# Optimization experiments

Measured on AMD Instinct MI355X. Metric: run time of the kernel, lower is better.

The kernel has to match this reference:

```python
import jax, jax.numpy as jnp
import numpy as np

NUM_EMBEDDINGS = 1024
EMBEDDING_DIM = 256
COMMITMENT_COST = 0.25
EPS_NORM = 1e-12  # F.normalize eps


def _l2_normalize(x, axis=-1):
    n = jnp.sqrt(jnp.sum(x * x, axis=axis, keepdims=True))
    return x / jnp.maximum(n, EPS_NORM)


def setup_inputs() -> dict:
    key = jax.random.key(0)
    k_in, k_w = jax.random.split(key)
    inputs = jax.random.normal(k_in, (16, 2048, 256), dtype=jnp.float32)
    # nn.Embedding weight initialized uniform(-1/K, 1/K)
    weight = jax.random.uniform(
        k_w, (NUM_EMBEDDINGS, EMBEDDING_DIM), dtype=jnp.float32,
        minval=-1.0 / NUM_EMBEDDINGS, maxval=1.0 / NUM_EMBEDDINGS)
    return {"inputs": inputs, "weight": weight}


def reference(inputs, weight):
    # inputs: [B, T, D]  weight: [K, D]
    B, T, D = inputs.shape
    K = weight.shape[0]

    x = jax.lax.stop_gradient(inputs)
    # cosine distance: normalized dot products  [B, T, K]
    distances = jnp.einsum(
        "btd,kd->btk", _l2_normalize(x), _l2_normalize(weight))

    encoding_indices = jnp.argmax(distances, axis=-1)            # [B, T]
    encodings = jax.nn.one_hot(encoding_indices, K, dtype=jnp.float32)  # [B, T, K]

    # one-hot matmul with codebook == gather
    quantized = jnp.take(weight, encoding_indices, axis=0)       # [B, T, D]

    e_latent_loss = COMMITMENT_COST * jnp.mean(
        (jax.lax.stop_gradient(quantized) - inputs) ** 2)
    q_latent_loss = jnp.mean((quantized - x) ** 2)

    # straight-through estimator
    quantized_st = inputs + jax.lax.stop_gradient(quantized - inputs)

    avg_probs = jnp.mean(encodings, axis=0)                      # [T, K]
    perplexity = jnp.exp(-jnp.sum(avg_probs * jnp.log(avg_probs + 1e-10)))

    # eval path (3D input): contra_loss = 0.0, no EMA/anchor update
    return (quantized_st,
            encoding_indices[..., None],
            q_latent_loss,
            e_latent_loss,
            perplexity,
            encodings)
```

## Files before the change

### kernel.cpp

```cpp
#include <hip/hip_runtime.h>
#include <math.h>
#include <float.h>

#define NUM_EMB   1024
#define DIM       256
#define BATCH     16
#define TLEN      2048
#define NTOK      (BATCH * TLEN)
#define QUANT_N   (NTOK * DIM)

#define QUANT_OFF 0
#define IDX_OFF   QUANT_N
#define QLOSS_OFF (IDX_OFF + NTOK)
#define ELOSS_OFF (QLOSS_OFF + 1)
#define PERP_OFF  (QLOSS_OFF + 2)
#define ENC_OFF   (QLOSS_OFF + 3)

typedef _Float16 f16;
typedef f16   f16x4 __attribute__((ext_vector_type(4)));
typedef f16   f16x8 __attribute__((ext_vector_type(8)));
typedef float f32x4 __attribute__((ext_vector_type(4)));

#define WS_XS_BYTE      0u
#define WS_WSP_BYTE     33554432u
#define WS_CNT_BYTE     34603008u
#define WS_WIN_BYTE     42991616u
#define WS_ACC_BYTE     43253760u
#define WS_NEED         (43253760u + 64u)

#define LWS_WHAT_BYTE   0
#define LWS_CNT_BYTE    1048576
#define LWS_ACC_BYTE    9437184

__device__ __forceinline__ void gl2lds16(const void* g, void* l) {
    __builtin_amdgcn_global_load_lds(
        (const __attribute__((address_space(1))) void*)g,
        (__attribute__((address_space(3))) void*)l, 16, 0, 0);
}


__global__ void k_zero_big(int4* __restrict__ counts4, int4* __restrict__ win4,
                           double* __restrict__ acc) {
    int i = blockIdx.x * blockDim.x + threadIdx.x;
    if (i < 524288) counts4[i] = make_int4(0, 0, 0, 0);
    else            win4[i - 524288] = make_int4(0, 0, 0, 0);
    if (i == 0) { acc[0] = 0.0; acc[1] = 0.0; }
}

__global__ void k_split_x(const float4* __restrict__ x4, f16* __restrict__ Xs) {
    int i = blockIdx.x * 256 + threadIdx.x;
    int row = i >> 6;
    int c4  = i & 63;
    float4 v = x4[i];
    f16 h0 = (f16)v.x, h1 = (f16)v.y, h2 = (f16)v.z, h3 = (f16)v.w;
    f16 l0 = (f16)(v.x - (float)h0), l1 = (f16)(v.y - (float)h1);
    f16 l2 = (f16)(v.z - (float)h2), l3 = (f16)(v.w - (float)h3);
    f16x4 hv = {h0, h1, h2, h3}, lv = {l0, l1, l2, l3};
    *(f16x4*)&Xs[(size_t)row * 512 + c4 * 4]       = hv;
    *(f16x4*)&Xs[(size_t)row * 512 + 256 + c4 * 4] = lv;
}

__global__ void k_norm_w_split(const float* __restrict__ w, f16* __restrict__ Ws) {
    int k = blockIdx.x;
    int lane = threadIdx.x;
    float4 v = ((const float4*)(w + (size_t)k * DIM))[lane];
    float ss = v.x * v.x + v.y * v.y + v.z * v.z + v.w * v.w;
    #pragma unroll
    for (int off = 32; off > 0; off >>= 1) ss += __shfl_down(ss, off);
    ss = __shfl(ss, 0);
    float denom = fmaxf(sqrtf(ss), 1e-12f);
    float a = v.x / denom, b = v.y / denom, c = v.z / denom, d = v.w / denom;
    f16 h0 = (f16)a, h1 = (f16)b, h2 = (f16)c, h3 = (f16)d;
    f16 l0 = (f16)(a - (float)h0), l1 = (f16)(b - (float)h1);
    f16 l2 = (f16)(c - (float)h2), l3 = (f16)(d - (float)h3);
    f16x4 hv = {h0, h1, h2, h3}, lv = {l0, l1, l2, l3};
    *(f16x4*)&Ws[(size_t)k * 512 + lane * 4]       = hv;
    *(f16x4*)&Ws[(size_t)k * 512 + 256 + lane * 4] = lv;
}

__global__ __launch_bounds__(256)
void k_gemm(const f16* __restrict__ Xs,
            const f16* __restrict__ Ws,
            unsigned long long* __restrict__ winners)
{
    __shared__ f16 As[128 * 32];
    __shared__ f16 Bs[128 * 32];
    __shared__ float redV[128][33];
    __shared__ int   redK[128][33];

    const int tid  = threadIdx.x;
    const int w    = tid >> 6, lane = tid & 63;
    const int tb   = blockIdx.x & 255;
    const int pg   = blockIdx.x >> 8;
    const int tok0 = tb * 128;
    const int wr   = w >> 1, wc = w & 1;
    const int quad = lane >> 4, l16 = lane & 15;

    const int stC0  = (w * 2) * 64 + lane;
    const int srow0 = stC0 >> 2, skc0 = (stC0 & 3) * 16;
    const int stC1  = stC0 + 64;
    const int srow1 = stC1 >> 2, skc1 = (stC1 & 3) * 16;

    for (int panel = 0; panel < 2; ++panel) {
        const int cw0 = (pg * 2 + panel) * 128;
        f32x4 acc[4][4];
        #pragma unroll
        for (int mi = 0; mi < 4; ++mi)
            #pragma unroll
            for (int ni = 0; ni < 4; ++ni)
                acc[mi][ni] = (f32x4){0.f, 0.f, 0.f, 0.f};

        const char* Xb = (const char*)Xs + (size_t)tok0 * 1024;
        const char* Wb = (const char*)Ws + (size_t)cw0 * 1024;

        for (int ks = 0; ks < 24; ++ks) {
            const int g = ks >> 3, r = ks & 7;
            const int akoff = ((g == 2) ? 512 : 0) + r * 64;
            const int bkoff = ((g == 1) ? 512 : 0) + r * 64;
            __syncthreads();
            gl2lds16(Xb + (size_t)srow0 * 1024 + akoff + skc0, (char*)As + (w * 2 + 0) * 1024);
            gl2lds16(Xb + (size_t)srow1 * 1024 + akoff + skc1, (char*)As + (w * 2 + 1) * 1024);
            gl2lds16(Wb + (size_t)srow0 * 1024 + bkoff + skc0, (char*)Bs + (w * 2 + 0) * 1024);
            gl2lds16(Wb + (size_t)srow1 * 1024 + bkoff + skc1, (char*)Bs + (w * 2 + 1) * 1024);
            __syncthreads();

            f16x8 af[4], bf[4];
            #pragma unroll
            for (int mi = 0; mi < 4; ++mi)
                af[mi] = *(const f16x8*)&As[(wr * 64 + mi * 16 + l16) * 32 + quad * 8];
            #pragma unroll
            for (int ni = 0; ni < 4; ++ni)
                bf[ni] = *(const f16x8*)&Bs[(wc * 64 + ni * 16 + l16) * 32 + quad * 8];
            #pragma unroll
            for (int mi = 0; mi < 4; ++mi)
                #pragma unroll
                for (int ni = 0; ni < 4; ++ni)
                    acc[mi][ni] = __builtin_amdgcn_mfma_f32_16x16x32_f16(
                        af[mi], bf[ni], acc[mi][ni], 0, 0, 0);
        }

        #pragma unroll
        for (int mi = 0; mi < 4; ++mi)
            #pragma unroll
            for (int rr = 0; rr < 4; ++rr) {
                float bv = acc[mi][0][rr]; int bk = cw0 + wc * 64 + l16;
                #pragma unroll
                for (int ni = 1; ni < 4; ++ni) {
                    float v = acc[mi][ni][rr];
                    int  kk = cw0 + wc * 64 + ni * 16 + l16;
                    if (v > bv) { bv = v; bk = kk; }
                }
                const int row = wr * 64 + mi * 16 + quad * 4 + rr;
                const int cg  = wc * 16 + l16;
                if (panel == 0) { redV[row][cg] = bv; redK[row][cg] = bk; }
                else if (bv > redV[row][cg]) { redV[row][cg] = bv; redK[row][cg] = bk; }
            }
    }
    __syncthreads();
    if (tid < 128) {
        float bv = redV[tid][0]; int bk = redK[tid][0];
        #pragma unroll 4
        for (int g2 = 1; g2 < 32; ++g2) {
            float v = redV[tid][g2]; int kk = redK[tid][g2];
            if (v > bv || (v == bv && kk < bk)) { bv = v; bk = kk; }
        }
        unsigned int ub = __float_as_uint(bv);
        ub = (ub & 0x80000000u) ? ~ub : (ub | 0x80000000u);
        unsigned long long key =
            ((unsigned long long)ub << 32) | (unsigned int)(1023 - bk);
        atomicMax(&winners[tok0 + tid], key);
    }
}

__global__ __launch_bounds__(256)
void k_epilogue(const float* __restrict__ x, const float* __restrict__ w,
                const unsigned long long* __restrict__ winners,
                float* __restrict__ out, int* __restrict__ counts,
                double* __restrict__ acc)
{
    const int wv = threadIdx.x >> 6, lane = threadIdx.x & 63;
    const int base = blockIdx.x * 32 + wv * 8;
    float mse = 0.0f;
    for (int t = 0; t < 8; ++t) {
        const int n = base + t;
        const int idx = 1023 - (int)(winners[n] & 1023u);
        float4 wvv = *(const float4*)(w + (size_t)idx * DIM + lane * 4);
        float4 xv  = *(const float4*)(x + (size_t)n * DIM + lane * 4);
        float dx = wvv.x - xv.x, dy = wvv.y - xv.y, dz = wvv.z - xv.z, dw2 = wvv.w - xv.w;
        mse += dx * dx + dy * dy + dz * dz + dw2 * dw2;
        *(float4*)(out + QUANT_OFF + (size_t)n * DIM + lane * 4) = wvv;
        if (lane == 0) {
            out[IDX_OFF + n] = (float)idx;
            atomicAdd(&counts[(n & (TLEN - 1)) * NUM_EMB + idx], 1);
        }
        float* enc = out + ENC_OFF + (size_t)n * NUM_EMB;
        #pragma unroll
        for (int s = 0; s < 4; ++s) {
            int kbase = s * 256 + lane * 4;
            float4 e;
            e.x = (kbase + 0 == idx) ? 1.0f : 0.0f;
            e.y = (kbase + 1 == idx) ? 1.0f : 0.0f;
            e.z = (kbase + 2 == idx) ? 1.0f : 0.0f;
            e.w = (kbase + 3 == idx) ? 1.0f : 0.0f;
            *(float4*)(enc + kbase) = e;
        }
    }
    #pragma unroll
    for (int off = 32; off > 0; off >>= 1) mse += __shfl_down(mse, off);
    if (lane == 0) atomicAdd(&acc[0], (double)mse);
}

__global__ void k_entropy(const int* __restrict__ counts, double* __restrict__ acc) {
    const int tid = blockIdx.x * blockDim.x + threadIdx.x;
    const int stride = gridDim.x * blockDim.x;
    float s = 0.0f;
    for (int e = tid; e < TLEN * NUM_EMB; e += stride) {
        int c = counts[e];
        if (c > 0) {
            float p = (float)c * 0.0625f;
            s += p * logf(p + 1e-10f);
        }
    }
    #pragma unroll
    for (int off = 32; off > 0; off >>= 1) s += __shfl_down(s, off);
    __shared__ float wsum[4];
    int lane = threadIdx.x & 63, wave = threadIdx.x >> 6;
    if (lane == 0) wsum[wave] = s;
    __syncthreads();
    if (threadIdx.x == 0) atomicAdd(&acc[1], (double)(wsum[0] + wsum[1] + wsum[2] + wsum[3]));
}

__global__ void k_final(const double* __restrict__ acc, float* __restrict__ out) {
    float mse_mean = (float)(acc[0] / (double)QUANT_N);
    out[QLOSS_OFF] = mse_mean;
    out[ELOSS_OFF] = 0.25f * mse_mean;
    float arg = -(float)acc[1];
    out[PERP_OFF] = (arg < 87.0f) ? expf(arg) : 3.0e38f;
}

__global__ void k_zero_legacy(int4* __restrict__ counts4, double* __restrict__ acc) {
    int i = blockIdx.x * blockDim.x + threadIdx.x;
    counts4[i] = make_int4(0, 0, 0, 0);
    if (i == 0) { acc[0] = 0.0; acc[1] = 0.0; }
}

__global__ void k_norm_w_legacy(const float* __restrict__ w, float* __restrict__ w_hat) {
    int k = blockIdx.x, lane = threadIdx.x;
    float4 v = ((const float4*)(w + (size_t)k * DIM))[lane];
    float ss = v.x * v.x + v.y * v.y + v.z * v.z + v.w * v.w;
    #pragma unroll
    for (int off = 32; off > 0; off >>= 1) ss += __shfl_down(ss, off);
    ss = __shfl(ss, 0);
    float denom = fmaxf(sqrtf(ss), 1e-12f);
    float4 o = {v.x / denom, v.y / denom, v.z / denom, v.w / denom};
    ((float4*)(w_hat + (size_t)k * DIM))[lane] = o;
}

#define BK 16
#define LDP 132
__global__ __launch_bounds__(256)
void k_main_legacy(const float* __restrict__ x, const float* __restrict__ w,
                   const float* __restrict__ w_hat, float* __restrict__ out,
                   int* __restrict__ counts, double* __restrict__ acc)
{
    __shared__ float As[BK][LDP];
    __shared__ float Bs[BK][LDP];
    __shared__ float redV[128][17];
    __shared__ int   redK[128][17];
    __shared__ int   sIdx[128];

    const int tid  = threadIdx.x;
    const int tok0 = blockIdx.x * 128;
    const int tr   = tid >> 4, tc = tid & 15;
    float rbestV = -3.0e30f; int rbestK = 0;
    const int strow = tid >> 2, stdq = tid & 3;

    for (int panel = 0; panel < 8; ++panel) {
        const int cw0 = panel * 128;
        float accs[8][8];
        #pragma unroll
        for (int i = 0; i < 8; ++i)
            #pragma unroll
            for (int j = 0; j < 8; ++j) accs[i][j] = 0.0f;
        for (int d0 = 0; d0 < DIM; d0 += BK) {
            __syncthreads();
            #pragma unroll
            for (int it = 0; it < 2; ++it) {
                int r = strow + it * 64;
                float4 a = *(const float4*)(x + (size_t)(tok0 + r) * DIM + d0 + stdq * 4);
                float4 b = *(const float4*)(w_hat + (size_t)(cw0 + r) * DIM + d0 + stdq * 4);
                As[stdq * 4 + 0][r] = a.x; As[stdq * 4 + 1][r] = a.y;
                As[stdq * 4 + 2][r] = a.z; As[stdq * 4 + 3][r] = a.w;
                Bs[stdq * 4 + 0][r] = b.x; Bs[stdq * 4 + 1][r] = b.y;
                Bs[stdq * 4 + 2][r] = b.z; Bs[stdq * 4 + 3][r] = b.w;
            }
            __syncthreads();
            #pragma unroll
            for (int kk = 0; kk < BK; ++kk) {
                float4 a0 = *(const float4*)&As[kk][tr * 8];
                float4 a1 = *(const float4*)&As[kk][tr * 8 + 4];
                float4 b0 = *(const float4*)&Bs[kk][tc * 8];
                float4 b1 = *(const float4*)&Bs[kk][tc * 8 + 4];
                float af[8] = {a0.x, a0.y, a0.z, a0.w, a1.x, a1.y, a1.z, a1.w};
                float bf[8] = {b0.x, b0.y, b0.z, b0.w, b1.x, b1.y, b1.z, b1.w};
                #pragma unroll
                for (int i = 0; i < 8; ++i)
                    #pragma unroll
                    for (int j = 0; j < 8; ++j)
                        accs[i][j] = fmaf(af[i], bf[j], accs[i][j]);
            }
        }
        #pragma unroll
        for (int i = 0; i < 8; ++i) {
            float bv = accs[i][0]; int bj = 0;
            #pragma unroll
            for (int j = 1; j < 8; ++j)
                if (accs[i][j] > bv) { bv = accs[i][j]; bj = j; }
            redV[tr * 8 + i][tc] = bv;
            redK[tr * 8 + i][tc] = cw0 + tc * 8 + bj;
        }
        __syncthreads();
        if (tid < 128) {
            #pragma unroll
            for (int g = 0; g < 16; ++g) {
                float v = redV[tid][g]; int kk2 = redK[tid][g];
                if (v > rbestV || (v == rbestV && kk2 < rbestK)) { rbestV = v; rbestK = kk2; }
            }
        }
        __syncthreads();
    }
    if (tid < 128) sIdx[tid] = rbestK;
    __syncthreads();

    const int wave = tid >> 6, lane = tid & 63;
    float mse = 0.0f;
    for (int tl = wave * 32; tl < wave * 32 + 32; ++tl) {
        const int n = tok0 + tl;
        const int idx = sIdx[tl];
        float4 wv = *(const float4*)(w + (size_t)idx * DIM + lane * 4);
        float4 xv = *(const float4*)(x + (size_t)n * DIM + lane * 4);
        float dx = wv.x - xv.x, dy = wv.y - xv.y, dz = wv.z - xv.z, dww = wv.w - xv.w;
        mse += dx * dx + dy * dy + dz * dz + dww * dww;
        *(float4*)(out + QUANT_OFF + (size_t)n * DIM + lane * 4) = wv;
        if (lane == 0) {
            out[IDX_OFF + n] = (float)idx;
            atomicAdd(&counts[(n & (TLEN - 1)) * NUM_EMB + idx], 1);
        }
        float* enc = out + ENC_OFF + (size_t)n * NUM_EMB;
        #pragma unroll
        for (int s = 0; s < 4; ++s) {
            int kbase = s * 256 + lane * 4;
            float4 e;
            e.x = (kbase + 0 == idx) ? 1.0f : 0.0f;
            e.y = (kbase + 1 == idx) ? 1.0f : 0.0f;
            e.z = (kbase + 2 == idx) ? 1.0f : 0.0f;
            e.w = (kbase + 3 == idx) ? 1.0f : 0.0f;
            *(float4*)(enc + kbase) = e;
        }
    }
    #pragma unroll
    for (int off = 32; off > 0; off >>= 1) mse += __shfl_down(mse, off);
    if (lane == 0) atomicAdd(&acc[0], (double)mse);
}

extern "C" void kernel_launch(void* const* d_in, const int* in_sizes, int n_in,
                              void* d_out, int out_size, void* d_ws, size_t ws_size,
                              hipStream_t stream) {
    const float* x = (const float*)d_in[0];
    const float* w = (const float*)d_in[1];
    float* out = (float*)d_out;

    if (ws_size >= WS_NEED) {
        f16*    Xs      = (f16*)((char*)d_ws + WS_XS_BYTE);
        f16*    Wsp     = (f16*)((char*)d_ws + WS_WSP_BYTE);
        int*    counts  = (int*)((char*)d_ws + WS_CNT_BYTE);
        unsigned long long* winners = (unsigned long long*)((char*)d_ws + WS_WIN_BYTE);
        double* acc     = (double*)((char*)d_ws + WS_ACC_BYTE);

        k_zero_big<<<2112, 256, 0, stream>>>((int4*)counts, (int4*)winners, acc);
        k_split_x<<<8192, 256, 0, stream>>>((const float4*)x, Xs);
        k_norm_w_split<<<NUM_EMB, 64, 0, stream>>>(w, Wsp);
        k_gemm<<<1024, 256, 0, stream>>>(Xs, Wsp, winners);
        k_epilogue<<<1024, 256, 0, stream>>>(x, w, winners, out, counts, acc);
        k_entropy<<<512, 256, 0, stream>>>(counts, acc);
        k_final<<<1, 1, 0, stream>>>(acc, out);
    } else {
        float*  w_hat  = (float*)((char*)d_ws + LWS_WHAT_BYTE);
        int*    counts = (int*)((char*)d_ws + LWS_CNT_BYTE);
        double* acc    = (double*)((char*)d_ws + LWS_ACC_BYTE);

        k_zero_legacy<<<2048, 256, 0, stream>>>((int4*)counts, acc);
        k_norm_w_legacy<<<NUM_EMB, 64, 0, stream>>>(w, w_hat);
        k_main_legacy<<<NTOK / 128, 256, 0, stream>>>(x, w, w_hat, out, counts, acc);
        k_entropy<<<512, 256, 0, stream>>>(counts, acc);
        k_final<<<1, 1, 0, stream>>>(acc, out);
    }
}
```

Measured before the change: 338.2 us.

## Restructure GEMM argmax: one panel per block, K=64 swizzled tiles, shuffle reduction

Result: no change. 335.6 us (-0.8%).

```diff
diff --git a/kernel.cpp b/kernel.cpp
--- a/kernel.cpp
+++ b/kernel.cpp
@@ -83,54 +83,65 @@
             const f16* __restrict__ Ws,
             unsigned long long* __restrict__ winners)
 {
-    __shared__ f16 As[128 * 32];
-    __shared__ f16 Bs[128 * 32];
-    __shared__ float redV[128][33];
-    __shared__ int   redK[128][33];
+    __shared__ f16 As[128 * 64];
+    __shared__ f16 Bs[128 * 64];
 
     const int tid  = threadIdx.x;
     const int w    = tid >> 6, lane = tid & 63;
     const int tb   = blockIdx.x & 255;
     const int pg   = blockIdx.x >> 8;
     const int tok0 = tb * 128;
+    const int cw0  = pg * 128;
     const int wr   = w >> 1, wc = w & 1;
     const int quad = lane >> 4, l16 = lane & 15;
 
-    const int stC0  = (w * 2) * 64 + lane;
-    const int srow0 = stC0 >> 2, skc0 = (stC0 & 3) * 16;
-    const int stC1  = stC0 + 64;
-    const int srow1 = stC1 >> 2, skc1 = (stC1 & 3) * 16;
-
-    for (int panel = 0; panel < 2; ++panel) {
-        const int cw0 = (pg * 2 + panel) * 128;
-        f32x4 acc[4][4];
-        #pragma unroll
-        for (int mi = 0; mi < 4; ++mi)
-            #pragma unroll
-            for (int ni = 0; ni < 4; ++ni)
-                acc[mi][ni] = (f32x4){0.f, 0.f, 0.f, 0.f};
-
-        const char* Xb = (const char*)Xs + (size_t)tok0 * 1024;
-        const char* Wb = (const char*)Ws + (size_t)cw0 * 1024;
-
-        for (int ks = 0; ks < 24; ++ks) {
-            const int g = ks >> 3, r = ks & 7;
-            const int akoff = ((g == 2) ? 512 : 0) + r * 64;
-            const int bkoff = ((g == 1) ? 512 : 0) + r * 64;
-            __syncthreads();
-            gl2lds16(Xb + (size_t)srow0 * 1024 + akoff + skc0, (char*)As + (w * 2 + 0) * 1024);
-            gl2lds16(Xb + (size_t)srow1 * 1024 + akoff + skc1, (char*)As + (w * 2 + 1) * 1024);
-            gl2lds16(Wb + (size_t)srow0 * 1024 + bkoff + skc0, (char*)Bs + (w * 2 + 0) * 1024);
-            gl2lds16(Wb + (size_t)srow1 * 1024 + bkoff + skc1, (char*)Bs + (w * 2 + 1) * 1024);
-            __syncthreads();
-
+    const char* Xb = (const char*)Xs + (size_t)tok0 * 1024;
+    const char* Wb = (const char*)Ws + (size_t)cw0 * 1024;
+
+    int srow[4], sgpart[4];
+    #pragma unroll
+    for (int j = 0; j < 4; ++j) {
+        int c = (w * 4 + j) * 64 + lane;
+        srow[j]   = c >> 3;
+        sgpart[j] = ((c & 7) ^ ((c >> 3) & 7)) * 16;
+    }
+
+    f32x4 acc[4][4];
+    #pragma unroll
+    for (int mi = 0; mi < 4; ++mi)
+        #pragma unroll
+        for (int ni = 0; ni < 4; ++ni)
+            acc[mi][ni] = (f32x4){0.f, 0.f, 0.f, 0.f};
+
+    for (int ks = 0; ks < 12; ++ks) {
+        const int g = ks >> 2, r = ks & 3;
+        const int akoff = ((g == 2) ? 512 : 0) + r * 128;
+        const int bkoff = ((g == 1) ? 512 : 0) + r * 128;
+        __syncthreads();
+        #pragma unroll
+        for (int j = 0; j < 4; ++j) {
+            gl2lds16(Xb + (size_t)srow[j] * 1024 + akoff + sgpart[j],
+                     (char*)As + (w * 4 + j) * 1024);
+            gl2lds16(Wb + (size_t)srow[j] * 1024 + bkoff + sgpart[j],
+                     (char*)Bs + (w * 4 + j) * 1024);
+        }
+        __syncthreads();
+
+        #pragma unroll
+        for (int ksub = 0; ksub < 2; ++ksub) {
             f16x8 af[4], bf[4];
             #pragma unroll
-            for (int mi = 0; mi < 4; ++mi)
-                af[mi] = *(const f16x8*)&As[(wr * 64 + mi * 16 + l16) * 32 + quad * 8];
-            #pragma unroll
-            for (int ni = 0; ni < 4; ++ni)
-                bf[ni] = *(const f16x8*)&Bs[(wc * 64 + ni * 16 + l16) * 32 + quad * 8];
+            for (int mi = 0; mi < 4; ++mi) {
+                const int m = wr * 64 + mi * 16 + l16;
+                const int slot = (quad + ksub * 4) ^ (l16 & 7);
+                af[mi] = *(const f16x8*)&As[m * 64 + slot * 8];
+            }
+            #pragma unroll
+            for (int ni = 0; ni < 4; ++ni) {
+                const int n = wc * 64 + ni * 16 + l16;
+                const int slot = (quad + ksub * 4) ^ (l16 & 7);
+                bf[ni] = *(const f16x8*)&Bs[n * 64 + slot * 8];
+            }
             #pragma unroll
             for (int mi = 0; mi < 4; ++mi)
                 #pragma unroll
@@ -138,37 +149,34 @@
                     acc[mi][ni] = __builtin_amdgcn_mfma_f32_16x16x32_f16(
                         af[mi], bf[ni], acc[mi][ni], 0, 0, 0);
         }
-
-        #pragma unroll
-        for (int mi = 0; mi < 4; ++mi)
-            #pragma unroll
-            for (int rr = 0; rr < 4; ++rr) {
-                float bv = acc[mi][0][rr]; int bk = cw0 + wc * 64 + l16;
-                #pragma unroll
-                for (int ni = 1; ni < 4; ++ni) {
-                    float v = acc[mi][ni][rr];
-                    int  kk = cw0 + wc * 64 + ni * 16 + l16;
-                    if (v > bv) { bv = v; bk = kk; }
-                }
+    }
+
+    #pragma unroll
+    for (int mi = 0; mi < 4; ++mi) {
+        #pragma unroll
+        for (int rr = 0; rr < 4; ++rr) {
+            float bv = acc[mi][0][rr];
+            int   bk = cw0 + wc * 64 + l16;
+            #pragma unroll
+            for (int ni = 1; ni < 4; ++ni) {
+                float v = acc[mi][ni][rr];
+                int  kk = cw0 + wc * 64 + ni * 16 + l16;
+                if (v > bv) { bv = v; bk = kk; }
+            }
+            unsigned int ub = __float_as_uint(bv);
+            ub = (ub & 0x80000000u) ? ~ub : (ub | 0x80000000u);
+            unsigned long long key =
+                ((unsigned long long)ub << 32) | (unsigned int)(1023 - bk);
+            #pragma unroll
+            for (int msk = 1; msk < 16; msk <<= 1) {
+                unsigned long long o = __shfl_xor(key, msk, 64);
+                if (o > key) key = o;
+            }
+            if (l16 == mi * 4 + rr) {
                 const int row = wr * 64 + mi * 16 + quad * 4 + rr;
-                const int cg  = wc * 16 + l16;
-                if (panel == 0) { redV[row][cg] = bv; redK[row][cg] = bk; }
-                else if (bv > redV[row][cg]) { redV[row][cg] = bv; redK[row][cg] = bk; }
-            }
-    }
-    __syncthreads();
-    if (tid < 128) {
-        float bv = redV[tid][0]; int bk = redK[tid][0];
-        #pragma unroll 4
-        for (int g2 = 1; g2 < 32; ++g2) {
-            float v = redV[tid][g2]; int kk = redK[tid][g2];
-            if (v > bv || (v == bv && kk < bk)) { bv = v; bk = kk; }
-        }
-        unsigned int ub = __float_as_uint(bv);
-        ub = (ub & 0x80000000u) ? ~ub : (ub | 0x80000000u);
-        unsigned long long key =
-            ((unsigned long long)ub << 32) | (unsigned int)(1023 - bk);
-        atomicMax(&winners[tok0 + tid], key);
+                atomicMax(&winners[tok0 + row], key);
+            }
+        }
     }
 }
 
@@ -380,7 +388,7 @@
         k_zero_big<<<2112, 256, 0, stream>>>((int4*)counts, (int4*)winners, acc);
         k_split_x<<<8192, 256, 0, stream>>>((const float4*)x, Xs);
         k_norm_w_split<<<NUM_EMB, 64, 0, stream>>>(w, Wsp);
-        k_gemm<<<1024, 256, 0, stream>>>(Xs, Wsp, winners);
+        k_gemm<<<2048, 256, 0, stream>>>(Xs, Wsp, winners);
         k_epilogue<<<1024, 256, 0, stream>>>(x, w, winners, out, counts, acc);
         k_entropy<<<512, 256, 0, stream>>>(counts, acc);
         k_final<<<1, 1, 0, stream>>>(acc, out);
```
